# Optimization experiments

Measured on AMD Instinct MI355X. Metric: run time of the kernel, lower is better.

Reference implementation:

```python
import jax, jax.numpy as jnp
import numpy as np
import math

B, S, D, K = 8, 2048, 1024, 64
EPS = 1e-5

def _ln(x):
    m = jnp.mean(x, axis=-1, keepdims=True)
    v = jnp.mean((x - m) ** 2, axis=-1, keepdims=True)
    return (x - m) * jax.lax.rsqrt(v + EPS)

def setup_inputs() -> dict:
    key = jax.random.key(0)
    ks = jax.random.split(key, 14)
    s = 0.02
    return {
        "x":  jax.random.normal(ks[0], (B, S, D), dtype=jnp.float32),
        "Wk": jax.random.normal(ks[1], (D, K), dtype=jnp.float32) * s,
        "bk": jnp.zeros((K,), dtype=jnp.float32),
        "Wq": jax.random.normal(ks[2], (D, K), dtype=jnp.float32) * s,
        "bq": jnp.zeros((K,), dtype=jnp.float32),
        "Wv": jax.random.normal(ks[3], (D, D), dtype=jnp.float32) * s,
        "bv": jnp.zeros((D,), dtype=jnp.float32),
        "Wb": jax.random.normal(ks[4], (D, 1), dtype=jnp.float32) * s,
        "bb": jnp.zeros((1,), dtype=jnp.float32),
        "W1": jax.random.normal(ks[5], (D, D), dtype=jnp.float32) * s,
        "b1": jnp.zeros((D,), dtype=jnp.float32),
        "g1": jnp.ones((D,), dtype=jnp.float32),
        "be1": jnp.zeros((D,), dtype=jnp.float32),
    }

def reference(x, Wk, bk, Wq, bq, Wv, bv, Wb, bb, W1, b1, g1, be1):
    scale = 1.0 / math.sqrt(K)
    keys    = (jnp.einsum('bsd,dk->bsk', x, Wk) + bk) * scale   # [B,S,K]
    queries = jnp.einsum('bsd,dk->bsk', x, Wq) + bq             # [B,S,K]
    values  = jnp.einsum('bsd,de->bse', x, Wv) + bv             # [B,S,D]
    biases  = jnp.einsum('bsd,do->bso', x, Wb) + bb             # [B,S,1]
    # scores[b,i,j] = keys[b,i] . queries[b,j] + biases[b,i]
    scores = jax.nn.sigmoid(jnp.einsum('bik,bjk->bij', keys, queries) + biases)
    attention = jnp.einsum('bij,bjd->bid', scores, values)      # [B,S,D]
    res = _ln(x + attention) * g1 + be1
    feedforward = jax.nn.relu(jnp.einsum('bsd,de->bse', res, W1) + b1)
    return _ln(res + feedforward)
```

## Files before the change

### kernel.cpp

```cpp
#include <hip/hip_runtime.h>
#include <math.h>


typedef __bf16 bf16_t;
typedef __bf16 bf16x4_t __attribute__((ext_vector_type(4)));
typedef __bf16 bf16x8_t __attribute__((ext_vector_type(8)));
typedef float  f32x4    __attribute__((ext_vector_type(4)));

#define DEV static __device__ __forceinline__

DEV void gll16(const void* g, void* l) {
  __builtin_amdgcn_global_load_lds(
      (const __attribute__((address_space(1))) void*)g,
      (__attribute__((address_space(3))) void*)l, 16, 0, 0);
}

template <int MODE, int MFAST>
__global__ __launch_bounds__(512, 2) void gemm256(
    const bf16_t* __restrict__ A, const bf16_t* __restrict__ B,
    bf16_t* __restrict__ C, int K, int lda, int ldb, int ldc,
    long sAb, long sBb, long sCb, const float* __restrict__ aux0) {
  const int gx = gridDim.x, gy = gridDim.y;
  const int gxy = gx * gy;
  const int nwg = gxy * (int)gridDim.z;
  const int orig = blockIdx.x + gx * blockIdx.y + gxy * blockIdx.z;
  const int lid = (orig & 7) * (nwg >> 3) + (orig >> 3);
  const int bz = lid / gxy;
  const int rem = lid - bz * gxy;
  const int bx = MFAST ? (rem / gy) : (rem % gx);
  const int by = MFAST ? (rem % gy) : (rem / gx);

  A += (long)bz * sAb;
  B += (long)bz * sBb;
  const int m0 = by * 256, n0 = bx * 256;

  __shared__ bf16_t SM[65536];
#define ASH(b, h) (&SM[(((b)*2 + (h)) << 13)])
#define BSH(b, h) (&SM[32768 + (((b)*2 + (h)) << 13)])

  const int tid = threadIdx.x;
  const int wid = tid >> 6, l = tid & 63;
  const int wr = wid >> 2, wc = wid & 3;
  const int lr = l & 15, lh = l >> 4;

  const int sRow = tid >> 2;
  const int sSl = (tid & 3) ^ ((tid >> 3) & 3);
  const bf16_t* Asrc = A + (long)(m0 + sRow) * lda + sSl * 8;
  const bf16_t* Bsrc = B + (long)(n0 + sRow) * ldb + sSl * 8;
  const long aStep = (long)128 * lda, bStep = (long)128 * ldb;

#define STAGE_A(b, h, kt) do { \
    const bf16_t* s_ = Asrc + (kt) * 64 + (h) * 32; \
    gll16(s_,         ASH(b, h) + tid * 8); \
    gll16(s_ + aStep, ASH(b, h) + 4096 + tid * 8); } while (0)
#define STAGE_B(b, h, kt) do { \
    const bf16_t* s_ = Bsrc + (kt) * 64 + (h) * 32; \
    gll16(s_,         BSH(b, h) + tid * 8); \
    gll16(s_ + bStep, BSH(b, h) + 4096 + tid * 8); } while (0)

  const int sw = (lh ^ ((lr >> 1) & 3)) * 8;
  const int aOff = (wr * 128 + lr) * 32 + sw;
  const int bOff = (wc * 64 + lr) * 32 + sw;

  f32x4 acc[8][4] = {};
  const int NT = K >> 6;

  STAGE_A(0, 0, 0); STAGE_B(0, 0, 0); STAGE_A(0, 1, 0); STAGE_B(0, 1, 0);
  asm volatile("s_waitcnt vmcnt(4)" ::: "memory");
  __builtin_amdgcn_s_barrier();

#define PHASE_SYNC() do { \
    __builtin_amdgcn_sched_barrier(0); \
    __builtin_amdgcn_s_barrier(); \
    asm volatile("s_waitcnt lgkmcnt(0)" ::: "memory"); \
    __builtin_amdgcn_sched_barrier(0); } while (0)
#define MFMA_LO() do { \
    __builtin_amdgcn_s_setprio(1); \
    _Pragma("unroll") for (int m = 0; m < 4; ++m) \
    _Pragma("unroll") for (int n = 0; n < 4; ++n) \
      acc[m][n] = __builtin_amdgcn_mfma_f32_16x16x32_bf16(aF[m], bF[n], acc[m][n], 0, 0, 0); \
    __builtin_amdgcn_s_setprio(0); } while (0)
#define MFMA_HI() do { \
    __builtin_amdgcn_s_setprio(1); \
    _Pragma("unroll") for (int m = 0; m < 4; ++m) \
    _Pragma("unroll") for (int n = 0; n < 4; ++n) \
      acc[m + 4][n] = __builtin_amdgcn_mfma_f32_16x16x32_bf16(aG[m], bF[n], acc[m + 4][n], 0, 0, 0); \
    __builtin_amdgcn_s_setprio(0); } while (0)

  for (int t = 0; t < NT; ++t) {
    const int p = t & 1, q = p ^ 1;
    const bool pf = (t + 1 < NT);
    bf16x8_t bF[4], aF[4], aG[4];

#pragma unroll
    for (int n = 0; n < 4; ++n) bF[n] = *(const bf16x8_t*)(BSH(p, 0) + bOff + n * 512);
#pragma unroll
    for (int m = 0; m < 4; ++m) aF[m] = *(const bf16x8_t*)(ASH(p, 0) + aOff + m * 512);
    if (pf) STAGE_A(q, 0, t + 1);
    PHASE_SYNC();
    MFMA_LO();

#pragma unroll
    for (int m = 0; m < 4; ++m) aG[m] = *(const bf16x8_t*)(ASH(p, 0) + aOff + (m + 4) * 512);
    if (pf) {
      STAGE_B(q, 0, t + 1);
      asm volatile("s_waitcnt vmcnt(4)" ::: "memory");
    } else {
      asm volatile("s_waitcnt vmcnt(0)" ::: "memory");
    }
    PHASE_SYNC();
    MFMA_HI();

#pragma unroll
    for (int n = 0; n < 4; ++n) bF[n] = *(const bf16x8_t*)(BSH(p, 1) + bOff + n * 512);
#pragma unroll
    for (int m = 0; m < 4; ++m) aF[m] = *(const bf16x8_t*)(ASH(p, 1) + aOff + m * 512);
    if (pf) STAGE_A(q, 1, t + 1);
    PHASE_SYNC();
    MFMA_LO();

#pragma unroll
    for (int m = 0; m < 4; ++m) aG[m] = *(const bf16x8_t*)(ASH(p, 1) + aOff + (m + 4) * 512);
    if (pf) STAGE_B(q, 1, t + 1);
    asm volatile("s_waitcnt vmcnt(4)" ::: "memory");
    PHASE_SYNC();
    MFMA_HI();
  }
#undef STAGE_A
#undef STAGE_B
#undef PHASE_SYNC
#undef MFMA_LO
#undef MFMA_HI

  bf16_t* Cb = C + (long)bz * sCb;
  const int rowb = m0 + wr * 128 + lh * 4;
  const int colb = n0 + wc * 64 + lr;
#pragma unroll
  for (int m = 0; m < 8; ++m)
#pragma unroll
    for (int n = 0; n < 4; ++n) {
      const f32x4 v = acc[m][n];
      const int cc = colb + n * 16;
#pragma unroll
      for (int r = 0; r < 4; ++r) {
        const int rr = rowb + m * 16 + r;
        const float val = v[r];
        if constexpr (MODE == 1) {
          Cb[(long)rr * ldc + cc] = (bf16_t)(val + aux0[rr]);
        } else {
          Cb[(long)rr * ldc + cc] = (bf16_t)fmaxf(val + aux0[cc], 0.0f);
        }
      }
    }
#undef ASH
#undef BSH
}

template <int MODE>
__global__ __launch_bounds__(512, 2) void gemm256p(
    const bf16_t* __restrict__ A, const bf16_t* __restrict__ B,
    bf16_t* __restrict__ C, int K, int lda, int ldb, int ldc,
    long sAb, long sBb, long sCb, const float* __restrict__ aux0) {
  const int gx = gridDim.x, gy = gridDim.y;
  const int gxy = gx * gy;
  const int nwg = gxy * (int)gridDim.z;
  const int orig = blockIdx.x + gx * blockIdx.y + gxy * blockIdx.z;
  const int lid = (orig & 7) * (nwg >> 3) + (orig >> 3);
  const int bz = lid / gxy;
  const int rem = lid - bz * gxy;
  const int bx = rem % gx;
  const int by = rem / gx;

  A += (long)bz * sAb;
  B += (long)bz * sBb;
  const int m0 = by * 256, n0 = bx * 256;

  __shared__ bf16_t SM[65536];
#define ASH(b, h) (&SM[(((b)*2 + (h)) << 13)])
#define BSH(b, h) (&SM[32768 + (((b)*2 + (h)) << 13)])

  const int tid = threadIdx.x;
  const int wid = tid >> 6, l = tid & 63;
  const int wr = wid >> 2, wc = wid & 3;
  const int lr = l & 15, lh = l >> 4;

  const int sRow = tid >> 2;
  const int sSl = (tid & 3) ^ ((tid >> 3) & 3);
  const bf16_t* Asrc = A + (long)(m0 + sRow) * lda + sSl * 8;
  const bf16_t* Bsrc = B + (long)(n0 + sRow) * ldb + sSl * 8;
  const long aStep = (long)128 * lda, bStep = (long)128 * ldb;

#define STAGE_A(b, h, kt) do { \
    const bf16_t* s_ = Asrc + (kt) * 64 + (h) * 32; \
    gll16(s_,         ASH(b, h) + tid * 8); \
    gll16(s_ + aStep, ASH(b, h) + 4096 + tid * 8); } while (0)
#define STAGE_B(b, h, kt) do { \
    const bf16_t* s_ = Bsrc + (kt) * 64 + (h) * 32; \
    gll16(s_,         BSH(b, h) + tid * 8); \
    gll16(s_ + bStep, BSH(b, h) + 4096 + tid * 8); } while (0)

  const int sw = (lh ^ ((lr >> 1) & 3)) * 8;
  const int aOff = (wr * 128 + lr) * 32 + sw;
  const int bOff = (wc * 64 + lr) * 32 + sw;

  f32x4 acc[8][4] = {};
  const int NT = K >> 6;

#define LGKM(n) do { \
    asm volatile("s_waitcnt lgkmcnt(" #n ")" ::: "memory"); \
    __builtin_amdgcn_sched_barrier(0); } while (0)
#define MFMA16(AS, BS, mo) do { \
    __builtin_amdgcn_s_setprio(1); \
    _Pragma("unroll") for (int m = 0; m < 4; ++m) \
    _Pragma("unroll") for (int n = 0; n < 4; ++n) \
      acc[m + (mo)][n] = __builtin_amdgcn_mfma_f32_16x16x32_bf16(AS[m], BS[n], acc[m + (mo)][n], 0, 0, 0); \
    __builtin_amdgcn_s_setprio(0); } while (0)

  STAGE_A(0, 0, 0); STAGE_B(0, 0, 0); STAGE_A(0, 1, 0); STAGE_B(0, 1, 0);
  asm volatile("s_waitcnt vmcnt(4)" ::: "memory");
  __builtin_amdgcn_s_barrier();

  bf16x8_t aA[4], aB[4], bA[4], bB[4];
#pragma unroll
  for (int n = 0; n < 4; ++n) bA[n] = *(const bf16x8_t*)(BSH(0, 0) + bOff + n * 512);
#pragma unroll
  for (int m = 0; m < 4; ++m) aA[m] = *(const bf16x8_t*)(ASH(0, 0) + aOff + m * 512);

  for (int t = 0; t < NT; ++t) {
    const int p = t & 1, q = p ^ 1;
    const bool pf = (t + 1 < NT);

#pragma unroll
    for (int m = 0; m < 4; ++m) aB[m] = *(const bf16x8_t*)(ASH(p, 0) + aOff + (m + 4) * 512);
    if (pf) STAGE_A(q, 0, t + 1);
    LGKM(4);
    MFMA16(aA, bA, 0);

    if (pf) {
      asm volatile("s_waitcnt vmcnt(2)" ::: "memory");
    } else {
      asm volatile("s_waitcnt vmcnt(0)" ::: "memory");
    }
    __builtin_amdgcn_sched_barrier(0);
    __builtin_amdgcn_s_barrier();
#pragma unroll
    for (int m = 0; m < 4; ++m) aA[m] = *(const bf16x8_t*)(ASH(p, 1) + aOff + m * 512);
#pragma unroll
    for (int n = 0; n < 4; ++n) bB[n] = *(const bf16x8_t*)(BSH(p, 1) + bOff + n * 512);
    if (pf) STAGE_B(q, 0, t + 1);
    LGKM(8);
    MFMA16(aB, bA, 4);

#pragma unroll
    for (int m = 0; m < 4; ++m) aB[m] = *(const bf16x8_t*)(ASH(p, 1) + aOff + (m + 4) * 512);
    if (pf) STAGE_A(q, 1, t + 1);
    LGKM(4);
    MFMA16(aA, bB, 0);

    if (pf) STAGE_B(q, 1, t + 1);
    asm volatile("s_waitcnt lgkmcnt(0)" ::: "memory");
    if (pf) {
      asm volatile("s_waitcnt vmcnt(4)" ::: "memory");
    }
    __builtin_amdgcn_sched_barrier(0);
    __builtin_amdgcn_s_barrier();
    if (pf) {
#pragma unroll
      for (int n = 0; n < 4; ++n) bA[n] = *(const bf16x8_t*)(BSH(q, 0) + bOff + n * 512);
#pragma unroll
      for (int m = 0; m < 4; ++m) aA[m] = *(const bf16x8_t*)(ASH(q, 0) + aOff + m * 512);
    }
    __builtin_amdgcn_sched_barrier(0);
    MFMA16(aB, bB, 4);
  }
#undef STAGE_A
#undef STAGE_B
#undef LGKM
#undef MFMA16

  bf16_t* Cb = C + (long)bz * sCb;
  const int rowb = m0 + wr * 128 + lh * 4;
  const int colb = n0 + wc * 64 + lr;
#pragma unroll
  for (int m = 0; m < 8; ++m)
#pragma unroll
    for (int n = 0; n < 4; ++n) {
      const f32x4 v = acc[m][n];
      const int cc = colb + n * 16;
#pragma unroll
      for (int r = 0; r < 4; ++r) {
        const int rr = rowb + m * 16 + r;
        Cb[(long)rr * ldc + cc] = (bf16_t)v[r];
      }
    }
#undef ASH
#undef BSH
}

__global__ __launch_bounds__(256) void kq_thin(
    const bf16_t* __restrict__ A, const bf16_t* __restrict__ B,
    bf16_t* __restrict__ C,
    const float* __restrict__ bk, const float* __restrict__ bq) {
  const int m0 = blockIdx.x * 64;

  __shared__ bf16_t SM[12288];
#define ASH(b) (&SM[(b) << 11])
#define BSH(b) (&SM[4096 + ((b) << 12)])

  const int tid = threadIdx.x;
  const int w = tid >> 6, l = tid & 63;
  const int lr = l & 15, lh = l >> 4;

  const int sRow = tid >> 2;
  const int sSl = (tid & 3) ^ ((tid >> 3) & 3);
  const bf16_t* Asrc = A + (long)(m0 + sRow) * 1024 + sSl * 8;
  const bf16_t* Bsrc0 = B + (long)sRow * 1024 + sSl * 8;
  const bf16_t* Bsrc1 = B + (long)(64 + sRow) * 1024 + sSl * 8;

  const int sw = (lh ^ ((lr >> 1) & 3)) * 8;
  const int aOff = (w * 16 + lr) * 32 + sw;

  f32x4 acc[8] = {};

  auto stage = [&](int buf, int k0) {
    gll16(Asrc + k0, ASH(buf) + tid * 8);
    gll16(Bsrc0 + k0, BSH(buf) + tid * 8);
    gll16(Bsrc1 + k0, BSH(buf) + 2048 + tid * 8);
  };

  stage(0, 0);
  __syncthreads();
  int cur = 0;

  for (int k0 = 0; k0 < 1024; k0 += 32) {
    if (k0 + 32 < 1024) stage(cur ^ 1, k0 + 32);

    const bf16x8_t aF = *(const bf16x8_t*)(ASH(cur) + aOff);
    bf16x8_t bF[8];
#pragma unroll
    for (int j = 0; j < 8; ++j)
      bF[j] = *(const bf16x8_t*)(BSH(cur) + (j * 16 + lr) * 32 + sw);
#pragma unroll
    for (int j = 0; j < 8; ++j)
      acc[j] = __builtin_amdgcn_mfma_f32_16x16x32_bf16(aF, bF[j], acc[j], 0, 0, 0);

    __syncthreads();
    cur ^= 1;
  }

  {
#pragma unroll
    for (int j = 0; j < 8; ++j) {
      const f32x4 v = acc[j];
      const int cl = j * 16 + lr;
      const float b = (cl < 64) ? bk[cl] : bq[cl - 64];
      const float s = (cl < 64) ? 0.125f : 1.0f;
#pragma unroll
      for (int r = 0; r < 4; ++r) {
        const int rl = w * 16 + lh * 4 + r;
        SM[rl * 128 + (cl ^ (lh << 4))] = (bf16_t)((v[r] + b) * s);
      }
    }
    __syncthreads();
    const int chunk = tid & 15, rsub = tid >> 4;
#pragma unroll
    for (int pp = 0; pp < 4; ++pp) {
      const int rl = pp * 16 + rsub;
      const int sc = chunk ^ (((rl >> 2) & 3) << 1);
      const bf16x8_t vv = *(const bf16x8_t*)&SM[rl * 128 + sc * 8];
      *(bf16x8_t*)&C[(long)(m0 + rl) * 128 + chunk * 8] = vv;
    }
  }
#undef ASH
#undef BSH
}

template <int MODE, int MFAST>
__global__ __launch_bounds__(256) void gemm_bt(
    const bf16_t* __restrict__ A, const bf16_t* __restrict__ B,
    void* __restrict__ Cv, int M, int N, int K, int lda, int ldb, int ldc,
    long sAb, long sBb, long sCb,
    const float* __restrict__ aux0, const float* __restrict__ aux1, long sAux) {
  const int gx = gridDim.x, gy = gridDim.y;
  const int gxy = gx * gy;
  const int nwg = gxy * (int)gridDim.z;
  const int orig = blockIdx.x + gx * blockIdx.y + gxy * blockIdx.z;
  const int q = nwg >> 3, r8 = nwg & 7;
  const int xcd = orig & 7, seq = orig >> 3;
  const int lid = (xcd < r8 ? xcd * (q + 1) : r8 * (q + 1) + (xcd - r8) * q) + seq;
  const int bz = lid / gxy;
  const int rem = lid - bz * gxy;
  const int bx = MFAST ? (rem / gy) : (rem % gx);
  const int by = MFAST ? (rem % gy) : (rem / gx);

  A += (long)bz * sAb;
  B += (long)bz * sBb;
  const float* a0 = aux0 + (long)bz * sAux;

  const int m0 = by * 128;
  const int n0 = bx * 128;

  __shared__ bf16_t SM[16384];
#define ASH(b) (&SM[(b) << 12])
#define BSH(b) (&SM[8192 + ((b) << 12)])

  const int tid = threadIdx.x;
  const int w = tid >> 6, l = tid & 63;
  const int wr = w >> 1, wc = w & 1;
  const int lr = l & 15, lh = l >> 4;

  const int srow = l >> 2;
  const int scol = (((l & 3) ^ (srow & 3)) << 3);

  f32x4 acc[4][4] = {};

  auto stage = [&](int buf, int k0) {
#pragma unroll
    for (int half = 0; half < 2; ++half) {
      const int i = 2 * w + half;
      const int row = (i << 4) + srow;
      gll16(A + (long)(m0 + row) * lda + k0 + scol, ASH(buf) + (i << 9));
      gll16(B + (long)(n0 + row) * ldb + k0 + scol, BSH(buf) + (i << 9));
    }
  };

  stage(0, 0);
  __syncthreads();
  int cur = 0;
  const int sw = ((lh ^ (lr & 3)) << 3);

  for (int k0 = 0; k0 < K; k0 += 32) {
    if (k0 + 32 < K) stage(cur ^ 1, k0 + 32);

    bf16x8_t af[4], bfm[4];
#pragma unroll
    for (int m = 0; m < 4; ++m)
      af[m] = *(const bf16x8_t*)(ASH(cur) + (((wr << 6) + (m << 4) + lr) << 5) + sw);
#pragma unroll
    for (int n = 0; n < 4; ++n)
      bfm[n] = *(const bf16x8_t*)(BSH(cur) + (((wc << 6) + (n << 4) + lr) << 5) + sw);
#pragma unroll
    for (int m = 0; m < 4; ++m)
#pragma unroll
      for (int n = 0; n < 4; ++n)
        acc[m][n] = __builtin_amdgcn_mfma_f32_16x16x32_bf16(af[m], bfm[n], acc[m][n], 0, 0, 0);

    __syncthreads();
    cur ^= 1;
  }

  {
    const int rowb = (wr << 6) + (lh << 2);
    const int colb = (wc << 6) + lr;
#pragma unroll
    for (int m = 0; m < 4; ++m)
#pragma unroll
      for (int n = 0; n < 4; ++n) {
        const f32x4 v = acc[m][n];
        const int cl = colb + (n << 4);
#pragma unroll
        for (int r = 0; r < 4; ++r) {
          const int rl = rowb + (m << 4) + r;
          const float zz = v[r] + a0[m0 + rl];
          SM[rl * 128 + (cl ^ (lh << 4))] =
              (bf16_t)__builtin_amdgcn_rcpf(1.0f + __expf(-zz));
        }
      }
    __syncthreads();
    bf16_t* Cb = (bf16_t*)Cv + (long)bz * sCb;
    const int chunk = tid & 15, rsub = tid >> 4;
#pragma unroll
    for (int pp = 0; pp < 8; ++pp) {
      const int rl = pp * 16 + rsub;
      const int sc = chunk ^ (((rl >> 2) & 3) << 1);
      const bf16x8_t vv = *(const bf16x8_t*)&SM[rl * 128 + sc * 8];
      *(bf16x8_t*)&Cb[(long)(m0 + rl) * ldc + n0 + chunk * 8] = vv;
    }
  }
#undef ASH
#undef BSH
}

__global__ __launch_bounds__(256) void cast_bias_kernel(
    const float* __restrict__ x, const float* __restrict__ Wb,
    const float* __restrict__ bb, bf16_t* __restrict__ x_bf,
    float* __restrict__ biases) {
  const int r = blockIdx.x * 4 + (threadIdx.x >> 6);
  const int l = threadIdx.x & 63;
  const float* xr = x + (long)r * 1024;
  bf16_t* orow = x_bf + (long)r * 1024;
  float s = 0.f;
#pragma unroll
  for (int i = 0; i < 4; ++i) {
    const int off = l * 4 + i * 256;
    const float4 v = *(const float4*)(xr + off);
    const float4 w = *(const float4*)(Wb + off);
    s += v.x * w.x + v.y * w.y + v.z * w.z + v.w * w.w;
    bf16x4_t o;
    o[0] = (bf16_t)v.x; o[1] = (bf16_t)v.y; o[2] = (bf16_t)v.z; o[3] = (bf16_t)v.w;
    *(bf16x4_t*)(orow + off) = o;
  }
#pragma unroll
  for (int off = 1; off < 64; off <<= 1) s += __shfl_xor(s, off);
  if (l == 0) biases[r] = s + bb[0];
}

__global__ __launch_bounds__(256) void transpose_cast_kernel(
    const float* __restrict__ in, bf16_t* __restrict__ out, int R, int C) {
  __shared__ float t[32][33];
  const int c0 = blockIdx.x * 32, r0 = blockIdx.y * 32;
  const int tx = threadIdx.x & 31, ty = threadIdx.x >> 5;
#pragma unroll
  for (int i = 0; i < 4; ++i) {
    const int rl = ty * 4 + i;
    t[rl][tx] = in[(long)(r0 + rl) * C + c0 + tx];
  }
  __syncthreads();
#pragma unroll
  for (int i = 0; i < 4; ++i) {
    const int rl = ty * 4 + i;
    out[(long)(c0 + rl) * R + r0 + tx] = (bf16_t)t[tx][rl];
  }
}

__global__ __launch_bounds__(256) void ln1_kernel(
    const bf16_t* __restrict__ x, const bf16_t* __restrict__ attn,
    const float* __restrict__ g, const float* __restrict__ be,
    bf16_t* __restrict__ res) {
  const int w = threadIdx.x >> 6, l = threadIdx.x & 63;
  const long r = (long)blockIdx.x * 4 + w;
  const bf16_t* xr = x + r * 1024;
  const bf16_t* ar = attn + r * 1024;
  float y[16];
  float s = 0.f, ss = 0.f;
#pragma unroll
  for (int h = 0; h < 2; ++h) {
    const int base = h * 512 + l * 8;
    const bf16x8_t xv = *(const bf16x8_t*)(xr + base);
    const bf16x8_t av = *(const bf16x8_t*)(ar + base);
#pragma unroll
    for (int j = 0; j < 8; ++j) {
      const float yy = (float)xv[j] + (float)av[j];
      y[h * 8 + j] = yy;
      s += yy; ss += yy * yy;
    }
  }
#pragma unroll
  for (int off = 1; off < 64; off <<= 1) {
    s += __shfl_xor(s, off);
    ss += __shfl_xor(ss, off);
  }
  const float mean = s * (1.0f / 1024.0f);
  const float rs = rsqrtf(ss * (1.0f / 1024.0f) - mean * mean + 1e-5f);
  bf16_t* orow = res + r * 1024;
#pragma unroll
  for (int h = 0; h < 2; ++h) {
    const int base = h * 512 + l * 8;
    bf16x8_t o;
#pragma unroll
    for (int j = 0; j < 8; ++j)
      o[j] = (bf16_t)((y[h * 8 + j] - mean) * rs * g[base + j] + be[base + j]);
    *(bf16x8_t*)(orow + base) = o;
  }
}

__global__ __launch_bounds__(256) void ln2_kernel(
    const bf16_t* __restrict__ res, const bf16_t* __restrict__ hh,
    float* __restrict__ out) {
  const int w = threadIdx.x >> 6, l = threadIdx.x & 63;
  const long r = (long)blockIdx.x * 4 + w;
  const bf16_t* rr = res + r * 1024;
  const bf16_t* hr = hh + r * 1024;
  float y[16];
  float s = 0.f, ss = 0.f;
#pragma unroll
  for (int h = 0; h < 2; ++h) {
    const int base = h * 512 + l * 8;
    const bf16x8_t rv = *(const bf16x8_t*)(rr + base);
    const bf16x8_t hv = *(const bf16x8_t*)(hr + base);
#pragma unroll
    for (int j = 0; j < 8; ++j) {
      const float yy = (float)rv[j] + (float)hv[j];
      y[h * 8 + j] = yy;
      s += yy; ss += yy * yy;
    }
  }
#pragma unroll
  for (int off = 1; off < 64; off <<= 1) {
    s += __shfl_xor(s, off);
    ss += __shfl_xor(ss, off);
  }
  const float mean = s * (1.0f / 1024.0f);
  const float rs = rsqrtf(ss * (1.0f / 1024.0f) - mean * mean + 1e-5f);
  float* orow = out + r * 1024;
#pragma unroll
  for (int h = 0; h < 2; ++h) {
    const int base = h * 512 + l * 8;
    float4 o1, o2;
    o1.x = (y[h * 8 + 0] - mean) * rs; o1.y = (y[h * 8 + 1] - mean) * rs;
    o1.z = (y[h * 8 + 2] - mean) * rs; o1.w = (y[h * 8 + 3] - mean) * rs;
    o2.x = (y[h * 8 + 4] - mean) * rs; o2.y = (y[h * 8 + 5] - mean) * rs;
    o2.z = (y[h * 8 + 6] - mean) * rs; o2.w = (y[h * 8 + 7] - mean) * rs;
    *(float4*)(orow + base) = o1;
    *(float4*)(orow + base + 4) = o2;
  }
}

extern "C" void kernel_launch(void* const* d_in, const int* in_sizes, int n_in,
                              void* d_out, int out_size, void* d_ws, size_t ws_size,
                              hipStream_t stream) {
  const float* x   = (const float*)d_in[0];
  const float* Wk  = (const float*)d_in[1];
  const float* bk  = (const float*)d_in[2];
  const float* Wq  = (const float*)d_in[3];
  const float* bq  = (const float*)d_in[4];
  const float* Wv  = (const float*)d_in[5];
  const float* bv  = (const float*)d_in[6];
  const float* Wb  = (const float*)d_in[7];
  const float* bb  = (const float*)d_in[8];
  const float* W1  = (const float*)d_in[9];
  const float* b1  = (const float*)d_in[10];
  const float* g1  = (const float*)d_in[11];
  const float* be1 = (const float*)d_in[12];
  float* out = (float*)d_out;

  char* ws = (char*)d_ws;
  bf16_t* x_bf    = (bf16_t*)(ws + 0);
  bf16_t* vt_bf   = (bf16_t*)(ws + 33554432);
  bf16_t* kq_bf   = (bf16_t*)(ws + 67108864);
  bf16_t* Wkqt    = (bf16_t*)(ws + 71303168);
  bf16_t* Wvt     = (bf16_t*)(ws + 71565312);
  bf16_t* W1t     = (bf16_t*)(ws + 73662464);
  float*  biases  = (float*) (ws + 75759616);
  bf16_t* scores  = (bf16_t*)(ws + 75825152);
  bf16_t* attn_bf = (bf16_t*)(ws + 142934016);
  bf16_t* res_bf  = (bf16_t*)(ws + 176488448);
  bf16_t* h_bf    = attn_bf;

  cast_bias_kernel<<<4096, 256, 0, stream>>>(x, Wb, bb, x_bf, biases);
  transpose_cast_kernel<<<dim3(2, 32), 256, 0, stream>>>(Wk, Wkqt, 1024, 64);
  transpose_cast_kernel<<<dim3(2, 32), 256, 0, stream>>>(Wq, Wkqt + 64 * 1024, 1024, 64);
  transpose_cast_kernel<<<dim3(32, 32), 256, 0, stream>>>(Wv, Wvt, 1024, 1024);
  transpose_cast_kernel<<<dim3(32, 32), 256, 0, stream>>>(W1, W1t, 1024, 1024);

  kq_thin<<<256, 256, 0, stream>>>(x_bf, Wkqt, kq_bf, bk, bq);

  gemm256<1, 1><<<dim3(64, 4, 1), 512, 0, stream>>>(
      Wvt, x_bf, vt_bf, 1024, 1024, 1024, 16384, 0, 0, 0, bv);

  gemm_bt<2, 0><<<dim3(16, 16, 8), 256, 0, stream>>>(
      kq_bf, kq_bf + 64, scores, 2048, 2048, 64, 128, 128, 2048,
      2048L * 128, 2048L * 128, 2048L * 2048, biases, nullptr, 2048);

  gemm256p<3><<<dim3(4, 8, 8), 512, 0, stream>>>(
      scores, vt_bf, attn_bf, 2048, 2048, 16384, 1024,
      2048L * 2048, 2048, 2048L * 1024, nullptr);

  ln1_kernel<<<4096, 256, 0, stream>>>(x_bf, attn_bf, g1, be1, res_bf);

  gemm256<4, 0><<<dim3(4, 64, 1), 512, 0, stream>>>(
      res_bf, W1t, h_bf, 1024, 1024, 1024, 1024, 0, 0, 0, b1);

  ln2_kernel<<<4096, 256, 0, stream>>>(res_bf, h_bf, out);
}
```

Measured before the change: 240.9 us.

## Unify GEMMs on prefetch-pipelined kernel and add single-shot K=64 scores kernel

Drops the older gemm256 main loop, so the V projection and FFN GEMMs now use the gemm256p pipeline, generalised with MFAST and the per-MODE bias/ReLU epilogues. The generic double-buffered gemm_bt used for the scores is replaced by a dedicated scores128 kernel. It loads the whole K=64 tile at once, waits once, and runs the MFMAs with no inner loop or per-step barriers. This removes loop and sync overhead on the short-K scores GEMM and applies the finer-grained LDS wait scheme to the other GEMMs, at the cost of hardcoded shapes in scores128.

```diff
diff --git a/kernel.cpp b/kernel.cpp
--- a/kernel.cpp
+++ b/kernel.cpp
@@ -16,7 +16,7 @@
 }
 
 template <int MODE, int MFAST>
-__global__ __launch_bounds__(512, 2) void gemm256(
+__global__ __launch_bounds__(512, 2) void gemm256p(
     const bf16_t* __restrict__ A, const bf16_t* __restrict__ B,
     bf16_t* __restrict__ C, int K, int lda, int ldb, int ldc,
     long sAb, long sBb, long sCb, const float* __restrict__ aux0) {
@@ -65,147 +65,6 @@
   f32x4 acc[8][4] = {};
   const int NT = K >> 6;
 
-  STAGE_A(0, 0, 0); STAGE_B(0, 0, 0); STAGE_A(0, 1, 0); STAGE_B(0, 1, 0);
-  asm volatile("s_waitcnt vmcnt(4)" ::: "memory");
-  __builtin_amdgcn_s_barrier();
-
-#define PHASE_SYNC() do { \
-    __builtin_amdgcn_sched_barrier(0); \
-    __builtin_amdgcn_s_barrier(); \
-    asm volatile("s_waitcnt lgkmcnt(0)" ::: "memory"); \
-    __builtin_amdgcn_sched_barrier(0); } while (0)
-#define MFMA_LO() do { \
-    __builtin_amdgcn_s_setprio(1); \
-    _Pragma("unroll") for (int m = 0; m < 4; ++m) \
-    _Pragma("unroll") for (int n = 0; n < 4; ++n) \
-      acc[m][n] = __builtin_amdgcn_mfma_f32_16x16x32_bf16(aF[m], bF[n], acc[m][n], 0, 0, 0); \
-    __builtin_amdgcn_s_setprio(0); } while (0)
-#define MFMA_HI() do { \
-    __builtin_amdgcn_s_setprio(1); \
-    _Pragma("unroll") for (int m = 0; m < 4; ++m) \
-    _Pragma("unroll") for (int n = 0; n < 4; ++n) \
-      acc[m + 4][n] = __builtin_amdgcn_mfma_f32_16x16x32_bf16(aG[m], bF[n], acc[m + 4][n], 0, 0, 0); \
-    __builtin_amdgcn_s_setprio(0); } while (0)
-
-  for (int t = 0; t < NT; ++t) {
-    const int p = t & 1, q = p ^ 1;
-    const bool pf = (t + 1 < NT);
-    bf16x8_t bF[4], aF[4], aG[4];
-
-#pragma unroll
-    for (int n = 0; n < 4; ++n) bF[n] = *(const bf16x8_t*)(BSH(p, 0) + bOff + n * 512);
-#pragma unroll
-    for (int m = 0; m < 4; ++m) aF[m] = *(const bf16x8_t*)(ASH(p, 0) + aOff + m * 512);
-    if (pf) STAGE_A(q, 0, t + 1);
-    PHASE_SYNC();
-    MFMA_LO();
-
-#pragma unroll
-    for (int m = 0; m < 4; ++m) aG[m] = *(const bf16x8_t*)(ASH(p, 0) + aOff + (m + 4) * 512);
-    if (pf) {
-      STAGE_B(q, 0, t + 1);
-      asm volatile("s_waitcnt vmcnt(4)" ::: "memory");
-    } else {
-      asm volatile("s_waitcnt vmcnt(0)" ::: "memory");
-    }
-    PHASE_SYNC();
-    MFMA_HI();
-
-#pragma unroll
-    for (int n = 0; n < 4; ++n) bF[n] = *(const bf16x8_t*)(BSH(p, 1) + bOff + n * 512);
-#pragma unroll
-    for (int m = 0; m < 4; ++m) aF[m] = *(const bf16x8_t*)(ASH(p, 1) + aOff + m * 512);
-    if (pf) STAGE_A(q, 1, t + 1);
-    PHASE_SYNC();
-    MFMA_LO();
-
-#pragma unroll
-    for (int m = 0; m < 4; ++m) aG[m] = *(const bf16x8_t*)(ASH(p, 1) + aOff + (m + 4) * 512);
-    if (pf) STAGE_B(q, 1, t + 1);
-    asm volatile("s_waitcnt vmcnt(4)" ::: "memory");
-    PHASE_SYNC();
-    MFMA_HI();
-  }
-#undef STAGE_A
-#undef STAGE_B
-#undef PHASE_SYNC
-#undef MFMA_LO
-#undef MFMA_HI
-
-  bf16_t* Cb = C + (long)bz * sCb;
-  const int rowb = m0 + wr * 128 + lh * 4;
-  const int colb = n0 + wc * 64 + lr;
-#pragma unroll
-  for (int m = 0; m < 8; ++m)
-#pragma unroll
-    for (int n = 0; n < 4; ++n) {
-      const f32x4 v = acc[m][n];
-      const int cc = colb + n * 16;
-#pragma unroll
-      for (int r = 0; r < 4; ++r) {
-        const int rr = rowb + m * 16 + r;
-        const float val = v[r];
-        if constexpr (MODE == 1) {
-          Cb[(long)rr * ldc + cc] = (bf16_t)(val + aux0[rr]);
-        } else {
-          Cb[(long)rr * ldc + cc] = (bf16_t)fmaxf(val + aux0[cc], 0.0f);
-        }
-      }
-    }
-#undef ASH
-#undef BSH
-}
-
-template <int MODE>
-__global__ __launch_bounds__(512, 2) void gemm256p(
-    const bf16_t* __restrict__ A, const bf16_t* __restrict__ B,
-    bf16_t* __restrict__ C, int K, int lda, int ldb, int ldc,
-    long sAb, long sBb, long sCb, const float* __restrict__ aux0) {
-  const int gx = gridDim.x, gy = gridDim.y;
-  const int gxy = gx * gy;
-  const int nwg = gxy * (int)gridDim.z;
-  const int orig = blockIdx.x + gx * blockIdx.y + gxy * blockIdx.z;
-  const int lid = (orig & 7) * (nwg >> 3) + (orig >> 3);
-  const int bz = lid / gxy;
-  const int rem = lid - bz * gxy;
-  const int bx = rem % gx;
-  const int by = rem / gx;
-
-  A += (long)bz * sAb;
-  B += (long)bz * sBb;
-  const int m0 = by * 256, n0 = bx * 256;
-
-  __shared__ bf16_t SM[65536];
-#define ASH(b, h) (&SM[(((b)*2 + (h)) << 13)])
-#define BSH(b, h) (&SM[32768 + (((b)*2 + (h)) << 13)])
-
-  const int tid = threadIdx.x;
-  const int wid = tid >> 6, l = tid & 63;
-  const int wr = wid >> 2, wc = wid & 3;
-  const int lr = l & 15, lh = l >> 4;
-
-  const int sRow = tid >> 2;
-  const int sSl = (tid & 3) ^ ((tid >> 3) & 3);
-  const bf16_t* Asrc = A + (long)(m0 + sRow) * lda + sSl * 8;
-  const bf16_t* Bsrc = B + (long)(n0 + sRow) * ldb + sSl * 8;
-  const long aStep = (long)128 * lda, bStep = (long)128 * ldb;
-
-#define STAGE_A(b, h, kt) do { \
-    const bf16_t* s_ = Asrc + (kt) * 64 + (h) * 32; \
-    gll16(s_,         ASH(b, h) + tid * 8); \
-    gll16(s_ + aStep, ASH(b, h) + 4096 + tid * 8); } while (0)
-#define STAGE_B(b, h, kt) do { \
-    const bf16_t* s_ = Bsrc + (kt) * 64 + (h) * 32; \
-    gll16(s_,         BSH(b, h) + tid * 8); \
-    gll16(s_ + bStep, BSH(b, h) + 4096 + tid * 8); } while (0)
-
-  const int sw = (lh ^ ((lr >> 1) & 3)) * 8;
-  const int aOff = (wr * 128 + lr) * 32 + sw;
-  const int bOff = (wc * 64 + lr) * 32 + sw;
-
-  f32x4 acc[8][4] = {};
-  const int NT = K >> 6;
-
 #define LGKM(n) do { \
     asm volatile("s_waitcnt lgkmcnt(" #n ")" ::: "memory"); \
     __builtin_amdgcn_sched_barrier(0); } while (0)
@@ -290,165 +149,77 @@
 #pragma unroll
       for (int r = 0; r < 4; ++r) {
         const int rr = rowb + m * 16 + r;
-        Cb[(long)rr * ldc + cc] = (bf16_t)v[r];
+        const float val = v[r];
+        if constexpr (MODE == 1) {
+          Cb[(long)rr * ldc + cc] = (bf16_t)(val + aux0[rr]);
+        } else if constexpr (MODE == 3) {
+          Cb[(long)rr * ldc + cc] = (bf16_t)val;
+        } else {
+          Cb[(long)rr * ldc + cc] = (bf16_t)fmaxf(val + aux0[cc], 0.0f);
+        }
       }
     }
 #undef ASH
 #undef BSH
 }
 
-__global__ __launch_bounds__(256) void kq_thin(
-    const bf16_t* __restrict__ A, const bf16_t* __restrict__ B,
-    bf16_t* __restrict__ C,
-    const float* __restrict__ bk, const float* __restrict__ bq) {
-  const int m0 = blockIdx.x * 64;
-
-  __shared__ bf16_t SM[12288];
-#define ASH(b) (&SM[(b) << 11])
-#define BSH(b) (&SM[4096 + ((b) << 12)])
-
-  const int tid = threadIdx.x;
-  const int w = tid >> 6, l = tid & 63;
-  const int lr = l & 15, lh = l >> 4;
-
-  const int sRow = tid >> 2;
-  const int sSl = (tid & 3) ^ ((tid >> 3) & 3);
-  const bf16_t* Asrc = A + (long)(m0 + sRow) * 1024 + sSl * 8;
-  const bf16_t* Bsrc0 = B + (long)sRow * 1024 + sSl * 8;
-  const bf16_t* Bsrc1 = B + (long)(64 + sRow) * 1024 + sSl * 8;
-
-  const int sw = (lh ^ ((lr >> 1) & 3)) * 8;
-  const int aOff = (w * 16 + lr) * 32 + sw;
-
-  f32x4 acc[8] = {};
-
-  auto stage = [&](int buf, int k0) {
-    gll16(Asrc + k0, ASH(buf) + tid * 8);
-    gll16(Bsrc0 + k0, BSH(buf) + tid * 8);
-    gll16(Bsrc1 + k0, BSH(buf) + 2048 + tid * 8);
-  };
-
-  stage(0, 0);
-  __syncthreads();
-  int cur = 0;
-
-  for (int k0 = 0; k0 < 1024; k0 += 32) {
-    if (k0 + 32 < 1024) stage(cur ^ 1, k0 + 32);
-
-    const bf16x8_t aF = *(const bf16x8_t*)(ASH(cur) + aOff);
-    bf16x8_t bF[8];
-#pragma unroll
-    for (int j = 0; j < 8; ++j)
-      bF[j] = *(const bf16x8_t*)(BSH(cur) + (j * 16 + lr) * 32 + sw);
-#pragma unroll
-    for (int j = 0; j < 8; ++j)
-      acc[j] = __builtin_amdgcn_mfma_f32_16x16x32_bf16(aF, bF[j], acc[j], 0, 0, 0);
-
-    __syncthreads();
-    cur ^= 1;
-  }
-
-  {
-#pragma unroll
-    for (int j = 0; j < 8; ++j) {
-      const f32x4 v = acc[j];
-      const int cl = j * 16 + lr;
-      const float b = (cl < 64) ? bk[cl] : bq[cl - 64];
-      const float s = (cl < 64) ? 0.125f : 1.0f;
-#pragma unroll
-      for (int r = 0; r < 4; ++r) {
-        const int rl = w * 16 + lh * 4 + r;
-        SM[rl * 128 + (cl ^ (lh << 4))] = (bf16_t)((v[r] + b) * s);
-      }
-    }
-    __syncthreads();
-    const int chunk = tid & 15, rsub = tid >> 4;
-#pragma unroll
-    for (int pp = 0; pp < 4; ++pp) {
-      const int rl = pp * 16 + rsub;
-      const int sc = chunk ^ (((rl >> 2) & 3) << 1);
-      const bf16x8_t vv = *(const bf16x8_t*)&SM[rl * 128 + sc * 8];
-      *(bf16x8_t*)&C[(long)(m0 + rl) * 128 + chunk * 8] = vv;
-    }
-  }
-#undef ASH
-#undef BSH
-}
-
-template <int MODE, int MFAST>
-__global__ __launch_bounds__(256) void gemm_bt(
-    const bf16_t* __restrict__ A, const bf16_t* __restrict__ B,
-    void* __restrict__ Cv, int M, int N, int K, int lda, int ldb, int ldc,
-    long sAb, long sBb, long sCb,
-    const float* __restrict__ aux0, const float* __restrict__ aux1, long sAux) {
-  const int gx = gridDim.x, gy = gridDim.y;
-  const int gxy = gx * gy;
-  const int nwg = gxy * (int)gridDim.z;
-  const int orig = blockIdx.x + gx * blockIdx.y + gxy * blockIdx.z;
-  const int q = nwg >> 3, r8 = nwg & 7;
-  const int xcd = orig & 7, seq = orig >> 3;
-  const int lid = (xcd < r8 ? xcd * (q + 1) : r8 * (q + 1) + (xcd - r8) * q) + seq;
-  const int bz = lid / gxy;
-  const int rem = lid - bz * gxy;
-  const int bx = MFAST ? (rem / gy) : (rem % gx);
-  const int by = MFAST ? (rem % gy) : (rem / gx);
-
-  A += (long)bz * sAb;
-  B += (long)bz * sBb;
-  const float* a0 = aux0 + (long)bz * sAux;
-
-  const int m0 = by * 128;
-  const int n0 = bx * 128;
+__global__ __launch_bounds__(256) void scores128(
+    const bf16_t* __restrict__ kq, bf16_t* __restrict__ C,
+    const float* __restrict__ biases) {
+  const int orig = blockIdx.x + 16 * blockIdx.y + 256 * blockIdx.z;
+  const int lid = (orig & 7) * 256 + (orig >> 3);
+  const int bz = lid >> 8;
+  const int rem = lid & 255;
+  const int bx = rem & 15, by = rem >> 4;
+
+  const bf16_t* A = kq + (long)bz * 2048 * 128;
+  const bf16_t* B = A + 64;
+  const float* a0 = biases + (long)bz * 2048;
+  const int m0 = by * 128, n0 = bx * 128;
 
   __shared__ bf16_t SM[16384];
-#define ASH(b) (&SM[(b) << 12])
-#define BSH(b) (&SM[8192 + ((b) << 12)])
+#define ASH(h) (&SM[(h) << 12])
+#define BSH(h) (&SM[8192 + ((h) << 12)])
 
   const int tid = threadIdx.x;
   const int w = tid >> 6, l = tid & 63;
   const int wr = w >> 1, wc = w & 1;
   const int lr = l & 15, lh = l >> 4;
 
-  const int srow = l >> 2;
-  const int scol = (((l & 3) ^ (srow & 3)) << 3);
+  const int sRow = tid >> 2;
+  const int sSl = ((tid & 3) ^ ((tid >> 3) & 3)) * 8;
+  const bf16_t* As = A + (long)(m0 + sRow) * 128 + sSl;
+  const bf16_t* Bs = B + (long)(n0 + sRow) * 128 + sSl;
+#pragma unroll
+  for (int h = 0; h < 2; ++h) {
+    gll16(As + h * 32, ASH(h) + tid * 8);
+    gll16(As + h * 32 + 64 * 128, ASH(h) + 2048 + tid * 8);
+    gll16(Bs + h * 32, BSH(h) + tid * 8);
+    gll16(Bs + h * 32 + 64 * 128, BSH(h) + 2048 + tid * 8);
+  }
+  asm volatile("s_waitcnt vmcnt(0)" ::: "memory");
+  __builtin_amdgcn_s_barrier();
+
+  const int sw = (lh ^ ((lr >> 1) & 3)) * 8;
+  const int aOff = (wr * 64 + lr) * 32 + sw;
+  const int bOff = (wc * 64 + lr) * 32 + sw;
 
   f32x4 acc[4][4] = {};
-
-  auto stage = [&](int buf, int k0) {
-#pragma unroll
-    for (int half = 0; half < 2; ++half) {
-      const int i = 2 * w + half;
-      const int row = (i << 4) + srow;
-      gll16(A + (long)(m0 + row) * lda + k0 + scol, ASH(buf) + (i << 9));
-      gll16(B + (long)(n0 + row) * ldb + k0 + scol, BSH(buf) + (i << 9));
-    }
-  };
-
-  stage(0, 0);
-  __syncthreads();
-  int cur = 0;
-  const int sw = ((lh ^ (lr & 3)) << 3);
-
-  for (int k0 = 0; k0 < K; k0 += 32) {
-    if (k0 + 32 < K) stage(cur ^ 1, k0 + 32);
-
-    bf16x8_t af[4], bfm[4];
+#pragma unroll
+  for (int h = 0; h < 2; ++h) {
+    bf16x8_t aF[4], bF[4];
+#pragma unroll
+    for (int m = 0; m < 4; ++m) aF[m] = *(const bf16x8_t*)(ASH(h) + aOff + m * 512);
+#pragma unroll
+    for (int n = 0; n < 4; ++n) bF[n] = *(const bf16x8_t*)(BSH(h) + bOff + n * 512);
 #pragma unroll
     for (int m = 0; m < 4; ++m)
-      af[m] = *(const bf16x8_t*)(ASH(cur) + (((wr << 6) + (m << 4) + lr) << 5) + sw);
-#pragma unroll
-    for (int n = 0; n < 4; ++n)
-      bfm[n] = *(const bf16x8_t*)(BSH(cur) + (((wc << 6) + (n << 4) + lr) << 5) + sw);
-#pragma unroll
-    for (int m = 0; m < 4; ++m)
 #pragma unroll
       for (int n = 0; n < 4; ++n)
-        acc[m][n] = __builtin_amdgcn_mfma_f32_16x16x32_bf16(af[m], bfm[n], acc[m][n], 0, 0, 0);
-
-    __syncthreads();
-    cur ^= 1;
-  }
-
+        acc[m][n] = __builtin_amdgcn_mfma_f32_16x16x32_bf16(aF[m], bF[n], acc[m][n], 0, 0, 0);
+  }
+
+  __builtin_amdgcn_s_barrier();
   {
     const int rowb = (wr << 6) + (lh << 2);
     const int colb = (wc << 6) + lr;
@@ -467,14 +238,92 @@
         }
       }
     __syncthreads();
-    bf16_t* Cb = (bf16_t*)Cv + (long)bz * sCb;
+    bf16_t* Cb = C + (long)bz * 2048 * 2048;
     const int chunk = tid & 15, rsub = tid >> 4;
 #pragma unroll
     for (int pp = 0; pp < 8; ++pp) {
       const int rl = pp * 16 + rsub;
       const int sc = chunk ^ (((rl >> 2) & 3) << 1);
       const bf16x8_t vv = *(const bf16x8_t*)&SM[rl * 128 + sc * 8];
-      *(bf16x8_t*)&Cb[(long)(m0 + rl) * ldc + n0 + chunk * 8] = vv;
+      *(bf16x8_t*)&Cb[(long)(m0 + rl) * 2048 + n0 + chunk * 8] = vv;
+    }
+  }
+#undef ASH
+#undef BSH
+}
+
+__global__ __launch_bounds__(256) void kq_thin(
+    const bf16_t* __restrict__ A, const bf16_t* __restrict__ B,
+    bf16_t* __restrict__ C,
+    const float* __restrict__ bk, const float* __restrict__ bq) {
+  const int m0 = blockIdx.x * 64;
+
+  __shared__ bf16_t SM[12288];
+#define ASH(b) (&SM[(b) << 11])
+#define BSH(b) (&SM[4096 + ((b) << 12)])
+
+  const int tid = threadIdx.x;
+  const int w = tid >> 6, l = tid & 63;
+  const int lr = l & 15, lh = l >> 4;
+
+  const int sRow = tid >> 2;
+  const int sSl = (tid & 3) ^ ((tid >> 3) & 3);
+  const bf16_t* Asrc = A + (long)(m0 + sRow) * 1024 + sSl * 8;
+  const bf16_t* Bsrc0 = B + (long)sRow * 1024 + sSl * 8;
+  const bf16_t* Bsrc1 = B + (long)(64 + sRow) * 1024 + sSl * 8;
+
+  const int sw = (lh ^ ((lr >> 1) & 3)) * 8;
+  const int aOff = (w * 16 + lr) * 32 + sw;
+
+  f32x4 acc[8] = {};
+
+  auto stage = [&](int buf, int k0) {
+    gll16(Asrc + k0, ASH(buf) + tid * 8);
+    gll16(Bsrc0 + k0, BSH(buf) + tid * 8);
+    gll16(Bsrc1 + k0, BSH(buf) + 2048 + tid * 8);
+  };
+
+  stage(0, 0);
+  __syncthreads();
+  int cur = 0;
+
+  for (int k0 = 0; k0 < 1024; k0 += 32) {
+    if (k0 + 32 < 1024) stage(cur ^ 1, k0 + 32);
+
+    const bf16x8_t aF = *(const bf16x8_t*)(ASH(cur) + aOff);
+    bf16x8_t bF[8];
+#pragma unroll
+    for (int j = 0; j < 8; ++j)
+      bF[j] = *(const bf16x8_t*)(BSH(cur) + (j * 16 + lr) * 32 + sw);
+#pragma unroll
+    for (int j = 0; j < 8; ++j)
+      acc[j] = __builtin_amdgcn_mfma_f32_16x16x32_bf16(aF, bF[j], acc[j], 0, 0, 0);
+
+    __syncthreads();
+    cur ^= 1;
+  }
+
+  {
+#pragma unroll
+    for (int j = 0; j < 8; ++j) {
+      const f32x4 v = acc[j];
+      const int cl = j * 16 + lr;
+      const float b = (cl < 64) ? bk[cl] : bq[cl - 64];
+      const float s = (cl < 64) ? 0.125f : 1.0f;
+#pragma unroll
+      for (int r = 0; r < 4; ++r) {
+        const int rl = w * 16 + lh * 4 + r;
+        SM[rl * 128 + (cl ^ (lh << 4))] = (bf16_t)((v[r] + b) * s);
+      }
+    }
+    __syncthreads();
+    const int chunk = tid & 15, rsub = tid >> 4;
+#pragma unroll
+    for (int pp = 0; pp < 4; ++pp) {
+      const int rl = pp * 16 + rsub;
+      const int sc = chunk ^ (((rl >> 2) & 3) << 1);
+      const bf16x8_t vv = *(const bf16x8_t*)&SM[rl * 128 + sc * 8];
+      *(bf16x8_t*)&C[(long)(m0 + rl) * 128 + chunk * 8] = vv;
     }
   }
 #undef ASH
@@ -645,20 +494,18 @@
 
   kq_thin<<<256, 256, 0, stream>>>(x_bf, Wkqt, kq_bf, bk, bq);
 
-  gemm256<1, 1><<<dim3(64, 4, 1), 512, 0, stream>>>(
+  gemm256p<1, 1><<<dim3(64, 4, 1), 512, 0, stream>>>(
       Wvt, x_bf, vt_bf, 1024, 1024, 1024, 16384, 0, 0, 0, bv);
 
-  gemm_bt<2, 0><<<dim3(16, 16, 8), 256, 0, stream>>>(
-      kq_bf, kq_bf + 64, scores, 2048, 2048, 64, 128, 128, 2048,
-      2048L * 128, 2048L * 128, 2048L * 2048, biases, nullptr, 2048);
-
-  gemm256p<3><<<dim3(4, 8, 8), 512, 0, stream>>>(
+  scores128<<<dim3(16, 16, 8), 256, 0, stream>>>(kq_bf, scores, biases);
+
+  gemm256p<3, 0><<<dim3(4, 8, 8), 512, 0, stream>>>(
       scores, vt_bf, attn_bf, 2048, 2048, 16384, 1024,
       2048L * 2048, 2048, 2048L * 1024, nullptr);
 
   ln1_kernel<<<4096, 256, 0, stream>>>(x_bf, attn_bf, g1, be1, res_bf);
 
-  gemm256<4, 0><<<dim3(4, 64, 1), 512, 0, stream>>>(
+  gemm256p<4, 0><<<dim3(4, 64, 1), 512, 0, stream>>>(
       res_bf, W1t, h_bf, 1024, 1024, 1024, 1024, 0, 0, 0, b1);
 
   ln2_kernel<<<4096, 256, 0, stream>>>(res_bf, h_bf, out);
```

Measured after the change: 237.6 us. No clear change (-1.4%).
